# Kernel tuning notes

Hardware: AMD Instinct MI355X
Metric: run time of the kernel (lower is better)

## Reference

```python
import jax, jax.numpy as jnp
import numpy as np

B, N, M = 64, 256, 16
ONF, OEF = 92, 41
NF, EF = 128, 64
FINAL = 128  # final_node_len; final_layer outputs FINAL//2


def _linear_params(key, fan_in, fan_out):
    # kaiming_uniform fan_in, relu: bound = sqrt(6/fan_in)
    bound = np.sqrt(6.0 / fan_in)
    W = jax.random.uniform(key, (fan_out, fan_in), jnp.float32, -bound, bound)
    b = jnp.zeros((fan_out,), jnp.float32)
    return W, b


def setup_inputs() -> dict:
    key = jax.random.key(0)
    ks = jax.random.split(key, 12)
    node_fea = jax.random.normal(ks[0], (B, N, ONF), jnp.float32)
    edge_fea = jax.random.normal(ks[1], (B, N, M, OEF), jnp.float32)
    edge_fea_idx = jax.random.randint(ks[2], (B, N, M), 0, N)
    dis = jax.random.uniform(ks[3], (N, N), jnp.float32)
    Wn, bn = _linear_params(ks[4], ONF, NF)
    We, be = _linear_params(ks[5], OEF, EF)
    W1, b1 = _linear_params(ks[6], 2 * NF + EF, 2 * NF)
    W2, b2 = _linear_params(ks[7], 2 * NF + EF, 2 * NF)
    W3, b3 = _linear_params(ks[8], 2 * NF + EF, 2 * NF)
    Wf, bf = _linear_params(ks[9], NF, FINAL // 2)
    return dict(node_fea=node_fea, edge_fea=edge_fea, edge_fea_idx=edge_fea_idx,
                dis=dis, Wn=Wn, bn=bn, We=We, be=be,
                W1=W1, b1=b1, a1=jnp.float32(0.7),
                W2=W2, b2=b2, a2=jnp.float32(0.7),
                W3=W3, b3=b3, a3=jnp.float32(0.7),
                Wf=Wf, bf=bf,
                DAw=jnp.float32(48.0 / 5.0), DAb=jnp.float32(-28.0 / 5.0))


def _conv(nf, ef, idx, W, b, alpha):
    # nf: [B,N,F]; ef: [B,N,M,E]; idx: [B,N,M]
    Bb, Nn, Mm = idx.shape
    F = nf.shape[-1]
    idx_c = jnp.maximum(idx, 0)
    gathered = jax.vmap(lambda x, i: x[i])(nf, idx_c)           # [B,N,M,F]
    self_exp = jnp.broadcast_to(nf[:, :, None, :], (Bb, Nn, Mm, F))
    total = jnp.concatenate([self_exp, gathered, ef], axis=-1)   # [B,N,M,2F+E]
    gated = jnp.einsum('bnmi,oi->bnmo', total, W) + b            # [B,N,M,2F]
    nbr_filter, nbr_core = jnp.split(gated, 2, axis=-1)
    mask = (idx >= 0).astype(nf.dtype)[..., None]
    nbr_filter = jax.nn.sigmoid(nbr_filter) * mask
    nbr_core = jax.nn.softplus(nbr_core)
    nbr_sumed = jnp.sum(nbr_filter * nbr_core, axis=2)           # [B,N,F]
    return jax.nn.softplus(alpha * nf + nbr_sumed)


def reference(node_fea, edge_fea, edge_fea_idx, dis,
              Wn, bn, We, be,
              W1, b1, a1, W2, b2, a2, W3, b3, a3,
              Wf, bf, DAw, DAb):
    nf = node_fea @ Wn.T + bn                                    # [B,N,NF]
    ef = edge_fea @ We.T + be                                    # [B,N,M,EF]
    nf = _conv(nf, ef, edge_fea_idx, W1, b1, a1)
    nf = _conv(nf, ef, edge_fea_idx, W2, b2, a2)
    nf = _conv(nf, ef, edge_fea_idx, W3, b3, a3)
    nf = nf @ Wf.T + bf                                          # [B,N,FINAL//2]
    DA = jax.nn.sigmoid(DAw * dis + DAb)                         # [N,N]
    node1 = jnp.einsum('ij,bjf->bif', DA, nf)
    return jnp.concatenate([nf, node1], axis=2)                  # [B,N,FINAL]
```

## Files before the change

kernel.cpp:

```cpp
#include <hip/hip_runtime.h>
#include <hip/hip_bf16.h>
#include <math.h>

#define Bb   64
#define Nn   256
#define Mm   16
#define ONF  92
#define OEF  41
#define NF   128
#define EF   64
#define KDIM 320
#define ODIM 256
#define FINAL 128
#define K0C  6

typedef __attribute__((ext_vector_type(8))) short short8;
typedef __attribute__((ext_vector_type(4))) float f32x4;

__device__ __forceinline__ float sigmoidf_(float x) {
    float e = __expf(-x);
    return __builtin_amdgcn_rcpf(1.0f + e);
}
__device__ __forceinline__ float softplusf_(float x) {
    return fmaxf(x, 0.0f) + __logf(1.0f + __expf(-fabsf(x)));
}
__device__ __forceinline__ __hip_bfloat16 to_bf16(float x) { return __float2bfloat16(x); }

__global__ void k_transpose(const float* __restrict__ in, float* __restrict__ out, int O, int I)
{
    int t = blockIdx.x * 256 + threadIdx.x;
    if (t < O * I) {
        int o = t / I, i = t - o * I;
        out[i * O + o] = in[t];
    }
}

__global__ void k_wswz2(const float* __restrict__ in, __hip_bfloat16* __restrict__ out,
                        int O, int Itot, int koff, int Kuse, int K0)
{
    int t = blockIdx.x * 256 + threadIdx.x;
    int total = (O >> 4) * K0 * 512;
    if (t < total) {
        int j = t & 7;
        int u = t >> 3;
        int lane = u & 63;
        int ln16 = lane & 15, q = lane >> 4;
        int v = u >> 6;
        int k0 = v % K0, tile = v / K0;
        int n = tile * 16 + ln16, k = k0 * 32 + q * 8 + j;
        out[t] = (k < Kuse) ? to_bf16(in[(size_t)n * Itot + koff + k]) : to_bf16(0.0f);
    }
}

__global__ void k_da(const float* __restrict__ dis, const float* __restrict__ pw,
                     const float* __restrict__ pb, __hip_bfloat16* __restrict__ DAf)
{
    int t = blockIdx.x * 256 + threadIdx.x;
    if (t < Nn * Nn) {
        int i = t >> 8, jx = t & 255;
        float v = sigmoidf_(fmaf(*pw, dis[t], *pb));
        int itile = i >> 4, ln16 = i & 15;
        int k0 = jx >> 5, q = (jx >> 3) & 3, jj = jx & 7;
        DAf[(size_t)((((itile * 8 + k0) << 6) + (q << 4) + ln16)) * 8 + jj] = to_bf16(v);
    }
}

template<int KIN, int K0, int NCOLS>
__global__ __launch_bounds__(256) void k_emb(
    const float* __restrict__ X, const __hip_bfloat16* __restrict__ Bswz,
    const float* __restrict__ bias, __hip_bfloat16* __restrict__ Y)
{
    constexpr int KP = K0 * 32;
    constexpr int TPW = NCOLS / 64;
    constexpr int OLD = NCOLS + 24;
    __shared__ __align__(16) __hip_bfloat16 A_s[4 * K0 * 512];
    __shared__ __align__(16) __hip_bfloat16 O_s[64 * OLD];

    const int row0 = blockIdx.x * 64;
    const int t = threadIdx.x;

    {
        const float4* Xb = (const float4*)(X + (size_t)row0 * KIN);
        constexpr int NV = (64 * KIN) / 4;
        for (int c = t; c < NV; c += 256) {
            float4 v = Xb[c];
            int flat = c * 4;
            #pragma unroll
            for (int e = 0; e < 4; e++) {
                int f = flat + e;
                int row = f / KIN, k = f - row * KIN;
                int mt = row >> 4, ln16 = row & 15;
                int k0 = k >> 5, q = (k >> 3) & 3, j = k & 7;
                float vv = (e == 0) ? v.x : (e == 1) ? v.y : (e == 2) ? v.z : v.w;
                A_s[(((mt * K0 + k0) << 6) + (q << 4) + ln16) * 8 + j] = to_bf16(vv);
            }
        }
        constexpr int PAD = KP - KIN;
        for (int c = t; c < 64 * PAD; c += 256) {
            int row = c / PAD, k = KIN + (c - row * PAD);
            int mt = row >> 4, ln16 = row & 15;
            int k0 = k >> 5, q = (k >> 3) & 3, j = k & 7;
            A_s[(((mt * K0 + k0) << 6) + (q << 4) + ln16) * 8 + j] = to_bf16(0.0f);
        }
    }
    __syncthreads();

    const int wv = t >> 6, lane = t & 63;
    const int q = lane >> 4, ln16 = lane & 15;

    f32x4 acc[4][TPW];
    #pragma unroll
    for (int p = 0; p < TPW; p++) {
        float bv = bias[(wv * TPW + p) * 16 + ln16];
        #pragma unroll
        for (int mt = 0; mt < 4; mt++) acc[mt][p] = (f32x4){bv, bv, bv, bv};
    }

    short8 bw[TPW][K0];
    #pragma unroll
    for (int p = 0; p < TPW; p++)
        #pragma unroll
        for (int k0 = 0; k0 < K0; k0++)
            bw[p][k0] = *(const short8*)(Bswz + ((size_t)((wv * TPW + p) * K0 + k0) << 9) + (lane << 3));

    #pragma unroll
    for (int k0 = 0; k0 < K0; k0++) {
        short8 af[4];
        #pragma unroll
        for (int mt = 0; mt < 4; mt++)
            af[mt] = *(const short8*)(A_s + (((mt * K0 + k0) << 6) + lane) * 8);
        #pragma unroll
        for (int mt = 0; mt < 4; mt++)
            #pragma unroll
            for (int p = 0; p < TPW; p++)
                acc[mt][p] = __builtin_amdgcn_mfma_f32_16x16x32_bf16(af[mt], bw[p][k0], acc[mt][p], 0, 0, 0);
    }

    #pragma unroll
    for (int mt = 0; mt < 4; mt++)
        #pragma unroll
        for (int p = 0; p < TPW; p++) {
            int col = (wv * TPW + p) * 16 + ln16;
            #pragma unroll
            for (int r = 0; r < 4; r++)
                O_s[(mt * 16 + q * 4 + r) * OLD + col] = to_bf16(acc[mt][p][r]);
        }
    __syncthreads();
    constexpr int CH = NCOLS / 8;
    for (int c = t; c < 64 * CH; c += 256) {
        int row = c / CH, ch = c - row * CH;
        *(uint4*)(Y + (size_t)(row0 + row) * NCOLS + ch * 8) =
            *(const uint4*)(O_s + row * OLD + ch * 8);
    }
}

__global__ __launch_bounds__(256) void k_self(
    const __hip_bfloat16* __restrict__ nf,
    const __hip_bfloat16* __restrict__ Wsb,
    const float* __restrict__ bias,
    float* __restrict__ S)
{
    __shared__ __align__(16) __hip_bfloat16 A_s[16 * 512];
    const int row0 = blockIdx.x * 64;
    const int t = threadIdx.x;
    const int wv = t >> 6, lane = t & 63;
    const int q = lane >> 4, ln16 = lane & 15;

    const __hip_bfloat16* rowp = nf + (size_t)(row0 + (wv << 4) + ln16) * NF;
    #pragma unroll
    for (int k0 = 0; k0 < 4; k0++)
        *(uint4*)(A_s + ((wv * 4 + k0) * 64 + lane) * 8) =
            *(const uint4*)(rowp + k0 * 32 + q * 8);
    __syncthreads();

    f32x4 acc[4][4];
    #pragma unroll
    for (int p = 0; p < 4; p++) {
        float bv = bias[(wv * 4 + p) * 16 + ln16];
        #pragma unroll
        for (int mt = 0; mt < 4; mt++) acc[mt][p] = (f32x4){bv, bv, bv, bv};
    }

    #pragma unroll
    for (int k0 = 0; k0 < 4; k0++) {
        short8 af[4];
        #pragma unroll
        for (int mt = 0; mt < 4; mt++)
            af[mt] = *(const short8*)(A_s + ((mt * 4 + k0) * 64 + lane) * 8);
        #pragma unroll
        for (int p = 0; p < 4; p++) {
            short8 bw = *(const short8*)(Wsb + ((size_t)((wv * 4 + p) * 4 + k0) << 9) + (lane << 3));
            #pragma unroll
            for (int mt = 0; mt < 4; mt++)
                acc[mt][p] = __builtin_amdgcn_mfma_f32_16x16x32_bf16(af[mt], bw, acc[mt][p], 0, 0, 0);
        }
    }

    #pragma unroll
    for (int mt = 0; mt < 4; mt++)
        #pragma unroll
        for (int p = 0; p < 4; p++) {
            int col = (wv * 4 + p) * 16 + ln16;
            #pragma unroll
            for (int r = 0; r < 4; r++)
                S[(size_t)(row0 + mt * 16 + q * 4 + r) * ODIM + col] = acc[mt][p][r];
        }
}

template<bool PRECOMP>
__global__ __launch_bounds__(256, 4) void k_conv_mfma(
    const __hip_bfloat16* __restrict__ nf_in,
    const float* __restrict__ edge_fea,
    const __hip_bfloat16* __restrict__ ef_bf,
    const int*   __restrict__ eidx,
    const float* __restrict__ WeT,
    const float* __restrict__ be,
    const __hip_bfloat16* __restrict__ Wb,
    const float* __restrict__ S,
    const float* __restrict__ palpha,
    __hip_bfloat16* __restrict__ nf_out)
{
    __shared__ __align__(16) __hip_bfloat16 A_s[4 * K0C * 512];

    const int node0 = blockIdx.x * 4;
    const int b = node0 >> 8;
    const int t = threadIdx.x;
    const int wv = t >> 6, lane = t & 63;
    const int q = lane >> 4, ln16 = lane & 15;
    const int row = (wv << 4) + ln16;

    const int myidx = eidx[node0 * Mm + row];
    const unsigned long long mball = __ballot(eidx[node0 * Mm + lane] >= 0);

    f32x4 accF[4][2], accC[4][2];
    #pragma unroll
    for (int mt = 0; mt < 4; mt++) {
        const float* Sp = S + (size_t)(node0 + mt) * ODIM;
        #pragma unroll
        for (int p = 0; p < 2; p++) {
            int colF = (2 * wv + p) * 16 + ln16;
            float sF = Sp[colF], sC = Sp[colF + NF];
            accF[mt][p] = (f32x4){sF, sF, sF, sF};
            accC[mt][p] = (f32x4){sC, sC, sC, sC};
        }
    }

    {
        int j = myidx < 0 ? 0 : myidx;
        const __hip_bfloat16* gathp = nf_in + (size_t)((b << 8) + j) * NF;
        #pragma unroll
        for (int k0 = 0; k0 < 4; k0++)
            *(uint4*)(A_s + ((wv * K0C + k0) * 64 + lane) * 8) =
                *(const uint4*)(gathp + k0 * 32 + q * 8);
        if (PRECOMP) {
            const __hip_bfloat16* efp = ef_bf + (size_t)((node0 << 4) + row) * EF;
            #pragma unroll
            for (int k0 = 0; k0 < 2; k0++)
                *(uint4*)(A_s + ((wv * K0C + 4 + k0) * 64 + lane) * 8) =
                    *(const uint4*)(efp + k0 * 32 + q * 8);
        } else {
            for (int c = t; c < 64 * EF; c += 256) {
                int rr = c >> 6, col = c & 63;
                float a = be[col];
                const float* er = edge_fea + (size_t)(node0 * Mm + rr) * OEF;
                #pragma unroll
                for (int i = 0; i < OEF; i++) a = fmaf(er[i], WeT[i * EF + col], a);
                int mt = rr >> 4, l16 = rr & 15;
                int k0 = 4 + (col >> 5), qq = (col >> 3) & 3, jj = col & 7;
                A_s[((mt * K0C + k0) * 64 + qq * 16 + l16) * 8 + jj] = to_bf16(a);
            }
        }
    }
    __syncthreads();

    const __hip_bfloat16* WF0 = Wb + ((size_t)(2 * wv) * (K0C * 512)) + (lane << 3);
    const __hip_bfloat16* WF1 = WF0 + K0C * 512;
    const __hip_bfloat16* WC0 = WF0 + 8 * (K0C * 512);
    const __hip_bfloat16* WC1 = WC0 + K0C * 512;

    #pragma unroll
    for (int k0 = 0; k0 < K0C; k0++) {
        short8 cF0 = *(const short8*)(WF0 + k0 * 512);
        short8 cF1 = *(const short8*)(WF1 + k0 * 512);
        short8 cC0 = *(const short8*)(WC0 + k0 * 512);
        short8 cC1 = *(const short8*)(WC1 + k0 * 512);
        short8 af[4];
        #pragma unroll
        for (int mt = 0; mt < 4; mt++)
            af[mt] = *(const short8*)(A_s + ((mt * K0C + k0) * 64 + lane) * 8);
        #pragma unroll
        for (int mt = 0; mt < 4; mt++) {
            accF[mt][0] = __builtin_amdgcn_mfma_f32_16x16x32_bf16(af[mt], cF0, accF[mt][0], 0, 0, 0);
            accF[mt][1] = __builtin_amdgcn_mfma_f32_16x16x32_bf16(af[mt], cF1, accF[mt][1], 0, 0, 0);
            accC[mt][0] = __builtin_amdgcn_mfma_f32_16x16x32_bf16(af[mt], cC0, accC[mt][0], 0, 0, 0);
            accC[mt][1] = __builtin_amdgcn_mfma_f32_16x16x32_bf16(af[mt], cC1, accC[mt][1], 0, 0, 0);
        }
    }

    const float alpha = *palpha;
    #pragma unroll
    for (int mt = 0; mt < 4; mt++) {
        const int gnode = node0 + mt;
        #pragma unroll
        for (int p = 0; p < 2; p++) {
            float partial = 0.0f;
            #pragma unroll
            for (int r = 0; r < 4; r++) {
                bool msk = (mball >> (mt * 16 + q * 4 + r)) & 1ull;
                float f = sigmoidf_(accF[mt][p][r]);
                float c = softplusf_(accC[mt][p][r]);
                partial += msk ? f * c : 0.0f;
            }
            partial += __shfl_xor(partial, 16);
            partial += __shfl_xor(partial, 32);
            if (q == 0) {
                int col = (2 * wv + p) * 16 + ln16;
                float self = __bfloat162float(nf_in[(size_t)gnode * NF + col]);
                nf_out[(size_t)gnode * NF + col] = to_bf16(softplusf_(fmaf(alpha, self, partial)));
            }
        }
    }
}

__global__ __launch_bounds__(256) void k_final_mfma(
    const __hip_bfloat16* __restrict__ nf, const __hip_bfloat16* __restrict__ Wfb,
    const float* __restrict__ bfv, float* __restrict__ out,
    __hip_bfloat16* __restrict__ XT)
{
    __shared__ __align__(16) __hip_bfloat16 A_s[16 * 512];
    const int node0 = blockIdx.x * 64;
    const int bloc = node0 >> 8;
    const int t = threadIdx.x;
    const int wv = t >> 6, lane = t & 63;
    const int q = lane >> 4, ln16 = lane & 15;

    const __hip_bfloat16* rowp = nf + (size_t)(node0 + (wv << 4) + ln16) * NF;
    #pragma unroll
    for (int k0 = 0; k0 < 4; k0++)
        *(uint4*)(A_s + ((wv * 4 + k0) * 64 + lane) * 8) =
            *(const uint4*)(rowp + k0 * 32 + q * 8);
    __syncthreads();

    short8 bw[4];
    #pragma unroll
    for (int k0 = 0; k0 < 4; k0++)
        bw[k0] = *(const short8*)(Wfb + ((size_t)(wv * 4 + k0) * 64 + lane) * 8);

    float bv = bfv[wv * 16 + ln16];
    f32x4 acc[4];
    #pragma unroll
    for (int mt = 0; mt < 4; mt++) acc[mt] = (f32x4){bv, bv, bv, bv};

    #pragma unroll
    for (int k0 = 0; k0 < 4; k0++) {
        short8 af[4];
        #pragma unroll
        for (int mt = 0; mt < 4; mt++)
            af[mt] = *(const short8*)(A_s + ((mt * 4 + k0) * 64 + lane) * 8);
        #pragma unroll
        for (int mt = 0; mt < 4; mt++)
            acc[mt] = __builtin_amdgcn_mfma_f32_16x16x32_bf16(af[mt], bw[k0], acc[mt], 0, 0, 0);
    }

    const int col = (wv << 4) + ln16;
    #pragma unroll
    for (int mt = 0; mt < 4; mt++)
        #pragma unroll
        for (int r = 0; r < 4; r++) {
            int row = mt * 16 + q * 4 + r;
            float v = acc[mt][r];
            out[(size_t)(node0 + row) * FINAL + col] = v;
            XT[(size_t)(bloc * 64 + col) * 256 + (node0 & 255) + row] = to_bf16(v);
        }
}

__global__ __launch_bounds__(256) void k_node1_mfma(
    const __hip_bfloat16* __restrict__ DAf,
    const __hip_bfloat16* __restrict__ XT,
    float* __restrict__ out)
{
    __shared__ __align__(16) __hip_bfloat16 B_s[32 * 512];
    const int blk = blockIdx.x;
    const int b = blk >> 2, i0 = (blk & 3) * 64;
    const int t = threadIdx.x;
    const int wv = t >> 6, lane = t & 63;
    const int q = lane >> 4, ln16 = lane & 15;

    const __hip_bfloat16* xrow = XT + (size_t)(b * 64 + (wv << 4) + ln16) * 256;
    #pragma unroll
    for (int k0 = 0; k0 < 8; k0++)
        *(uint4*)(B_s + ((wv * 8 + k0) * 64 + lane) * 8) =
            *(const uint4*)(xrow + k0 * 32 + q * 8);
    __syncthreads();

    f32x4 acc[4];
    #pragma unroll
    for (int mt = 0; mt < 4; mt++) acc[mt] = (f32x4){0.f, 0.f, 0.f, 0.f};

    #pragma unroll
    for (int k0 = 0; k0 < 8; k0++) {
        short8 bfr = *(const short8*)(B_s + ((wv * 8 + k0) * 64 + lane) * 8);
        short8 af[4];
        #pragma unroll
        for (int mt = 0; mt < 4; mt++)
            af[mt] = *(const short8*)(DAf + (size_t)(((i0 >> 4) + mt) * 8 + k0) * 512 + (lane << 3));
        #pragma unroll
        for (int mt = 0; mt < 4; mt++)
            acc[mt] = __builtin_amdgcn_mfma_f32_16x16x32_bf16(af[mt], bfr, acc[mt], 0, 0, 0);
    }

    #pragma unroll
    for (int mt = 0; mt < 4; mt++)
        #pragma unroll
        for (int r = 0; r < 4; r++) {
            int i = i0 + mt * 16 + q * 4 + r;
            out[(size_t)((b << 8) + i) * FINAL + 64 + (wv << 4) + ln16] = acc[mt][r];
        }
}

extern "C" void kernel_launch(void* const* d_in, const int* in_sizes, int n_in,
                              void* d_out, int out_size, void* d_ws, size_t ws_size,
                              hipStream_t stream)
{
    const float* node_fea = (const float*)d_in[0];
    const float* edge_fea = (const float*)d_in[1];
    const int*   eidx     = (const int*)  d_in[2];
    const float* dis      = (const float*)d_in[3];
    const float* Wn = (const float*)d_in[4];
    const float* bn = (const float*)d_in[5];
    const float* We = (const float*)d_in[6];
    const float* be = (const float*)d_in[7];
    const float* W1 = (const float*)d_in[8];
    const float* b1 = (const float*)d_in[9];
    const float* a1 = (const float*)d_in[10];
    const float* W2 = (const float*)d_in[11];
    const float* b2 = (const float*)d_in[12];
    const float* a2 = (const float*)d_in[13];
    const float* W3 = (const float*)d_in[14];
    const float* b3 = (const float*)d_in[15];
    const float* a3 = (const float*)d_in[16];
    const float* Wf = (const float*)d_in[17];
    const float* bf = (const float*)d_in[18];
    const float* DAw = (const float*)d_in[19];
    const float* DAb = (const float*)d_in[20];
    float* out = (float*)d_out;

    char* base = (char*)d_ws;
    size_t off = 0;
    auto alloc = [&](size_t bytes) { char* p = base + off; off = (off + bytes + 255) & ~(size_t)255; return p; };
    __hip_bfloat16* nfA = (__hip_bfloat16*)alloc((size_t)Bb * Nn * NF * 2);
    __hip_bfloat16* nfB = (__hip_bfloat16*)alloc((size_t)Bb * Nn * NF * 2);
    __hip_bfloat16* W1b = (__hip_bfloat16*)alloc((size_t)16 * K0C * 512 * 2);
    __hip_bfloat16* W2b = (__hip_bfloat16*)alloc((size_t)16 * K0C * 512 * 2);
    __hip_bfloat16* W3b = (__hip_bfloat16*)alloc((size_t)16 * K0C * 512 * 2);
    __hip_bfloat16* W1s = (__hip_bfloat16*)alloc((size_t)16 * 4 * 512 * 2);
    __hip_bfloat16* W2s = (__hip_bfloat16*)alloc((size_t)16 * 4 * 512 * 2);
    __hip_bfloat16* W3s = (__hip_bfloat16*)alloc((size_t)16 * 4 * 512 * 2);
    float* WeT = (float*)alloc((size_t)OEF * EF * 4);
    __hip_bfloat16* DAf = (__hip_bfloat16*)alloc((size_t)Nn * Nn * 2);
    __hip_bfloat16* Wnb = (__hip_bfloat16*)alloc((size_t)(NF / 16) * 3 * 512 * 2);
    __hip_bfloat16* Web = (__hip_bfloat16*)alloc((size_t)(EF / 16) * 2 * 512 * 2);
    __hip_bfloat16* Wfb = (__hip_bfloat16*)alloc((size_t)(64 / 16) * 4 * 512 * 2);
    __hip_bfloat16* XT  = (__hip_bfloat16*)alloc((size_t)Bb * 64 * Nn * 2);
    float* S = (float*)alloc((size_t)Bb * Nn * ODIM * 4);
    __hip_bfloat16* efb = (__hip_bfloat16*)alloc((size_t)Bb * Nn * Mm * EF * 2);
    const bool precomp = (ws_size >= off);

    hipLaunchKernelGGL(k_transpose, dim3((EF * OEF + 255) / 256), dim3(256), 0, stream, We, WeT, EF, OEF);
    hipLaunchKernelGGL(k_wswz2, dim3((16 * K0C * 512 + 255) / 256), dim3(256), 0, stream, W1, W1b, ODIM, KDIM, NF, 192, K0C);
    hipLaunchKernelGGL(k_wswz2, dim3((16 * K0C * 512 + 255) / 256), dim3(256), 0, stream, W2, W2b, ODIM, KDIM, NF, 192, K0C);
    hipLaunchKernelGGL(k_wswz2, dim3((16 * K0C * 512 + 255) / 256), dim3(256), 0, stream, W3, W3b, ODIM, KDIM, NF, 192, K0C);
    hipLaunchKernelGGL(k_wswz2, dim3((16 * 4 * 512 + 255) / 256), dim3(256), 0, stream, W1, W1s, ODIM, KDIM, 0, NF, 4);
    hipLaunchKernelGGL(k_wswz2, dim3((16 * 4 * 512 + 255) / 256), dim3(256), 0, stream, W2, W2s, ODIM, KDIM, 0, NF, 4);
    hipLaunchKernelGGL(k_wswz2, dim3((16 * 4 * 512 + 255) / 256), dim3(256), 0, stream, W3, W3s, ODIM, KDIM, 0, NF, 4);
    hipLaunchKernelGGL(k_wswz2, dim3((8 * 3 * 512 + 255) / 256), dim3(256), 0, stream, Wn, Wnb, NF, ONF, 0, ONF, 3);
    hipLaunchKernelGGL(k_wswz2, dim3((4 * 2 * 512 + 255) / 256), dim3(256), 0, stream, We, Web, EF, OEF, 0, OEF, 2);
    hipLaunchKernelGGL(k_wswz2, dim3((4 * 4 * 512 + 255) / 256), dim3(256), 0, stream, Wf, Wfb, 64, NF, 0, NF, 4);
    hipLaunchKernelGGL(k_da, dim3((Nn * Nn + 255) / 256), dim3(256), 0, stream, dis, DAw, DAb, DAf);

    if (precomp)
        hipLaunchKernelGGL((k_emb<OEF, 2, EF>), dim3(Bb * Nn * Mm / 64), dim3(256), 0, stream,
                           edge_fea, Web, be, efb);
    hipLaunchKernelGGL((k_emb<ONF, 3, NF>), dim3(Bb * Nn / 64), dim3(256), 0, stream,
                       node_fea, Wnb, bn, nfA);

    const int NG = Bb * Nn / 64;
    if (precomp) {
        hipLaunchKernelGGL(k_self, dim3(NG), dim3(256), 0, stream, nfA, W1s, b1, S);
        hipLaunchKernelGGL((k_conv_mfma<true>), dim3(Bb * Nn / 4), dim3(256), 0, stream,
                           nfA, edge_fea, efb, eidx, WeT, be, W1b, S, a1, nfB);
        hipLaunchKernelGGL(k_self, dim3(NG), dim3(256), 0, stream, nfB, W2s, b2, S);
        hipLaunchKernelGGL((k_conv_mfma<true>), dim3(Bb * Nn / 4), dim3(256), 0, stream,
                           nfB, edge_fea, efb, eidx, WeT, be, W2b, S, a2, nfA);
        hipLaunchKernelGGL(k_self, dim3(NG), dim3(256), 0, stream, nfA, W3s, b3, S);
        hipLaunchKernelGGL((k_conv_mfma<true>), dim3(Bb * Nn / 4), dim3(256), 0, stream,
                           nfA, edge_fea, efb, eidx, WeT, be, W3b, S, a3, nfB);
    } else {
        hipLaunchKernelGGL(k_self, dim3(NG), dim3(256), 0, stream, nfA, W1s, b1, S);
        hipLaunchKernelGGL((k_conv_mfma<false>), dim3(Bb * Nn / 4), dim3(256), 0, stream,
                           nfA, edge_fea, efb, eidx, WeT, be, W1b, S, a1, nfB);
        hipLaunchKernelGGL(k_self, dim3(NG), dim3(256), 0, stream, nfB, W2s, b2, S);
        hipLaunchKernelGGL((k_conv_mfma<false>), dim3(Bb * Nn / 4), dim3(256), 0, stream,
                           nfB, edge_fea, efb, eidx, WeT, be, W2b, S, a2, nfA);
        hipLaunchKernelGGL(k_self, dim3(NG), dim3(256), 0, stream, nfA, W3s, b3, S);
        hipLaunchKernelGGL((k_conv_mfma<false>), dim3(Bb * Nn / 4), dim3(256), 0, stream,
                           nfA, edge_fea, efb, eidx, WeT, be, W3b, S, a3, nfB);
    }

    hipLaunchKernelGGL(k_final_mfma, dim3(Bb * Nn / 64), dim3(256), 0, stream, nfB, Wfb, bf, out, XT);
    hipLaunchKernelGGL(k_node1_mfma, dim3(Bb * 4), dim3(256), 0, stream, DAf, XT, out);
}
```

Measured before the change: 344.7 us.

## Fuse self-term GEMM into conv kernel and merge prep/embed launches

Removes the separate k_self kernel and its fp32 S buffer. Each conv block now computes its own 4 nodes' self-projection with extra MFMAs on a padded 16-row tile and broadcasts the results via shuffles. All weight-swizzle, transpose and DA prep kernels are merged into one k_prep launch, and the node and edge embedding kernels into one k_embed_all launch, which cuts launch count and S traffic. The self GEMM in conv uses only 4 of 16 MFMA rows, so it wastes compute, and launch bounds drop from 4 to 3 blocks per CU, which may reduce occupancy.

```diff
diff --git a/kernel.cpp b/kernel.cpp
--- a/kernel.cpp
+++ b/kernel.cpp
@@ -26,37 +26,65 @@
 }
 __device__ __forceinline__ __hip_bfloat16 to_bf16(float x) { return __float2bfloat16(x); }
 
-__global__ void k_transpose(const float* __restrict__ in, float* __restrict__ out, int O, int I)
+__device__ __forceinline__ void swz(const float* __restrict__ in, __hip_bfloat16* __restrict__ out,
+                                    int t, int Itot, int koff, int Kuse, int K0)
+{
+    int j = t & 7;
+    int u = t >> 3;
+    int lane = u & 63;
+    int ln16 = lane & 15, q = lane >> 4;
+    int v = u >> 6;
+    int k0 = v % K0, tile = v / K0;
+    int n = tile * 16 + ln16, k = k0 * 32 + q * 8 + j;
+    out[t] = (k < Kuse) ? to_bf16(in[(size_t)n * Itot + koff + k]) : to_bf16(0.0f);
+}
+
+#define SZ_WET (OEF * EF)
+#define SZ_WB  (16 * K0C * 512)
+#define SZ_WS  (16 * 4 * 512)
+#define SZ_WNB ((NF / 16) * 3 * 512)
+#define SZ_WEB ((EF / 16) * 2 * 512)
+#define SZ_WFB ((64 / 16) * 4 * 512)
+#define SZ_DA  (Nn * Nn)
+#define PREP_TOTAL (SZ_WET + 3 * SZ_WB + 3 * SZ_WS + SZ_WNB + SZ_WEB + SZ_WFB + SZ_DA)
+
+__global__ __launch_bounds__(256) void k_prep(
+    const float* __restrict__ We, const float* __restrict__ W1,
+    const float* __restrict__ W2, const float* __restrict__ W3,
+    const float* __restrict__ Wn, const float* __restrict__ Wf,
+    const float* __restrict__ dis, const float* __restrict__ pw, const float* __restrict__ pb,
+    float* __restrict__ WeT,
+    __hip_bfloat16* __restrict__ W1b, __hip_bfloat16* __restrict__ W2b, __hip_bfloat16* __restrict__ W3b,
+    __hip_bfloat16* __restrict__ W1s, __hip_bfloat16* __restrict__ W2s, __hip_bfloat16* __restrict__ W3s,
+    __hip_bfloat16* __restrict__ Wnb, __hip_bfloat16* __restrict__ Web, __hip_bfloat16* __restrict__ Wfb,
+    __hip_bfloat16* __restrict__ DAf)
 {
     int t = blockIdx.x * 256 + threadIdx.x;
-    if (t < O * I) {
-        int o = t / I, i = t - o * I;
-        out[i * O + o] = in[t];
-    }
-}
-
-__global__ void k_wswz2(const float* __restrict__ in, __hip_bfloat16* __restrict__ out,
-                        int O, int Itot, int koff, int Kuse, int K0)
-{
-    int t = blockIdx.x * 256 + threadIdx.x;
-    int total = (O >> 4) * K0 * 512;
-    if (t < total) {
-        int j = t & 7;
-        int u = t >> 3;
-        int lane = u & 63;
-        int ln16 = lane & 15, q = lane >> 4;
-        int v = u >> 6;
-        int k0 = v % K0, tile = v / K0;
-        int n = tile * 16 + ln16, k = k0 * 32 + q * 8 + j;
-        out[t] = (k < Kuse) ? to_bf16(in[(size_t)n * Itot + koff + k]) : to_bf16(0.0f);
-    }
-}
-
-__global__ void k_da(const float* __restrict__ dis, const float* __restrict__ pw,
-                     const float* __restrict__ pb, __hip_bfloat16* __restrict__ DAf)
-{
-    int t = blockIdx.x * 256 + threadIdx.x;
-    if (t < Nn * Nn) {
+    if (t < SZ_WET) {
+        int o = t / OEF, i = t - o * OEF;
+        WeT[i * EF + o] = We[t];
+        return;
+    }
+    t -= SZ_WET;
+    if (t < SZ_WB) { swz(W1, W1b, t, KDIM, NF, 192, K0C); return; }
+    t -= SZ_WB;
+    if (t < SZ_WB) { swz(W2, W2b, t, KDIM, NF, 192, K0C); return; }
+    t -= SZ_WB;
+    if (t < SZ_WB) { swz(W3, W3b, t, KDIM, NF, 192, K0C); return; }
+    t -= SZ_WB;
+    if (t < SZ_WS) { swz(W1, W1s, t, KDIM, 0, NF, 4); return; }
+    t -= SZ_WS;
+    if (t < SZ_WS) { swz(W2, W2s, t, KDIM, 0, NF, 4); return; }
+    t -= SZ_WS;
+    if (t < SZ_WS) { swz(W3, W3s, t, KDIM, 0, NF, 4); return; }
+    t -= SZ_WS;
+    if (t < SZ_WNB) { swz(Wn, Wnb, t, ONF, 0, ONF, 3); return; }
+    t -= SZ_WNB;
+    if (t < SZ_WEB) { swz(We, Web, t, OEF, 0, OEF, 2); return; }
+    t -= SZ_WEB;
+    if (t < SZ_WFB) { swz(Wf, Wfb, t, NF, 0, NF, 4); return; }
+    t -= SZ_WFB;
+    if (t < SZ_DA) {
         int i = t >> 8, jx = t & 255;
         float v = sigmoidf_(fmaf(*pw, dis[t], *pb));
         int itile = i >> 4, ln16 = i & 15;
@@ -66,17 +94,16 @@
 }
 
 template<int KIN, int K0, int NCOLS>
-__global__ __launch_bounds__(256) void k_emb(
-    const float* __restrict__ X, const __hip_bfloat16* __restrict__ Bswz,
-    const float* __restrict__ bias, __hip_bfloat16* __restrict__ Y)
+__device__ __forceinline__ void emb_body(
+    int bid, const float* __restrict__ X, const __hip_bfloat16* __restrict__ Bswz,
+    const float* __restrict__ bias, __hip_bfloat16* __restrict__ Y,
+    __hip_bfloat16* A_s, __hip_bfloat16* O_s)
 {
     constexpr int KP = K0 * 32;
     constexpr int TPW = NCOLS / 64;
     constexpr int OLD = NCOLS + 24;
-    __shared__ __align__(16) __hip_bfloat16 A_s[4 * K0 * 512];
-    __shared__ __align__(16) __hip_bfloat16 O_s[64 * OLD];
-
-    const int row0 = blockIdx.x * 64;
+
+    const int row0 = bid * 64;
     const int t = threadIdx.x;
 
     {
@@ -154,61 +181,22 @@
     }
 }
 
-__global__ __launch_bounds__(256) void k_self(
-    const __hip_bfloat16* __restrict__ nf,
-    const __hip_bfloat16* __restrict__ Wsb,
-    const float* __restrict__ bias,
-    float* __restrict__ S)
-{
-    __shared__ __align__(16) __hip_bfloat16 A_s[16 * 512];
-    const int row0 = blockIdx.x * 64;
-    const int t = threadIdx.x;
-    const int wv = t >> 6, lane = t & 63;
-    const int q = lane >> 4, ln16 = lane & 15;
-
-    const __hip_bfloat16* rowp = nf + (size_t)(row0 + (wv << 4) + ln16) * NF;
-    #pragma unroll
-    for (int k0 = 0; k0 < 4; k0++)
-        *(uint4*)(A_s + ((wv * 4 + k0) * 64 + lane) * 8) =
-            *(const uint4*)(rowp + k0 * 32 + q * 8);
-    __syncthreads();
-
-    f32x4 acc[4][4];
-    #pragma unroll
-    for (int p = 0; p < 4; p++) {
-        float bv = bias[(wv * 4 + p) * 16 + ln16];
-        #pragma unroll
-        for (int mt = 0; mt < 4; mt++) acc[mt][p] = (f32x4){bv, bv, bv, bv};
-    }
-
-    #pragma unroll
-    for (int k0 = 0; k0 < 4; k0++) {
-        short8 af[4];
-        #pragma unroll
-        for (int mt = 0; mt < 4; mt++)
-            af[mt] = *(const short8*)(A_s + ((mt * 4 + k0) * 64 + lane) * 8);
-        #pragma unroll
-        for (int p = 0; p < 4; p++) {
-            short8 bw = *(const short8*)(Wsb + ((size_t)((wv * 4 + p) * 4 + k0) << 9) + (lane << 3));
-            #pragma unroll
-            for (int mt = 0; mt < 4; mt++)
-                acc[mt][p] = __builtin_amdgcn_mfma_f32_16x16x32_bf16(af[mt], bw, acc[mt][p], 0, 0, 0);
-        }
-    }
-
-    #pragma unroll
-    for (int mt = 0; mt < 4; mt++)
-        #pragma unroll
-        for (int p = 0; p < 4; p++) {
-            int col = (wv * 4 + p) * 16 + ln16;
-            #pragma unroll
-            for (int r = 0; r < 4; r++)
-                S[(size_t)(row0 + mt * 16 + q * 4 + r) * ODIM + col] = acc[mt][p][r];
-        }
+__global__ __launch_bounds__(256) void k_embed_all(
+    const float* __restrict__ node_fea, const __hip_bfloat16* __restrict__ Wnb,
+    const float* __restrict__ bn, __hip_bfloat16* __restrict__ nf0,
+    const float* __restrict__ edge_fea, const __hip_bfloat16* __restrict__ Web,
+    const float* __restrict__ be, __hip_bfloat16* __restrict__ efb)
+{
+    __shared__ __align__(16) __hip_bfloat16 A_s[4 * 3 * 512];
+    __shared__ __align__(16) __hip_bfloat16 O_s[64 * (NF + 24)];
+    if (blockIdx.x < 256)
+        emb_body<ONF, 3, NF>(blockIdx.x, node_fea, Wnb, bn, nf0, A_s, O_s);
+    else
+        emb_body<OEF, 2, EF>(blockIdx.x - 256, edge_fea, Web, be, efb, A_s, O_s);
 }
 
 template<bool PRECOMP>
-__global__ __launch_bounds__(256, 4) void k_conv_mfma(
+__global__ __launch_bounds__(256, 3) void k_conv_mfma(
     const __hip_bfloat16* __restrict__ nf_in,
     const float* __restrict__ edge_fea,
     const __hip_bfloat16* __restrict__ ef_bf,
@@ -216,11 +204,13 @@
     const float* __restrict__ WeT,
     const float* __restrict__ be,
     const __hip_bfloat16* __restrict__ Wb,
-    const float* __restrict__ S,
+    const __hip_bfloat16* __restrict__ Wsb,
+    const float* __restrict__ bias,
     const float* __restrict__ palpha,
     __hip_bfloat16* __restrict__ nf_out)
 {
     __shared__ __align__(16) __hip_bfloat16 A_s[4 * K0C * 512];
+    __shared__ __align__(16) __hip_bfloat16 A_sf[4 * 512];
 
     const int node0 = blockIdx.x * 4;
     const int b = node0 >> 8;
@@ -232,19 +222,6 @@
     const int myidx = eidx[node0 * Mm + row];
     const unsigned long long mball = __ballot(eidx[node0 * Mm + lane] >= 0);
 
-    f32x4 accF[4][2], accC[4][2];
-    #pragma unroll
-    for (int mt = 0; mt < 4; mt++) {
-        const float* Sp = S + (size_t)(node0 + mt) * ODIM;
-        #pragma unroll
-        for (int p = 0; p < 2; p++) {
-            int colF = (2 * wv + p) * 16 + ln16;
-            float sF = Sp[colF], sC = Sp[colF + NF];
-            accF[mt][p] = (f32x4){sF, sF, sF, sF};
-            accC[mt][p] = (f32x4){sC, sC, sC, sC};
-        }
-    }
-
     {
         int j = myidx < 0 ? 0 : myidx;
         const __hip_bfloat16* gathp = nf_in + (size_t)((b << 8) + j) * NF;
@@ -252,6 +229,9 @@
         for (int k0 = 0; k0 < 4; k0++)
             *(uint4*)(A_s + ((wv * K0C + k0) * 64 + lane) * 8) =
                 *(const uint4*)(gathp + k0 * 32 + q * 8);
+        if (lane < 16)
+            *(uint4*)(A_sf + (((lane >> 2) * 64) + (lane & 3) * 16 + wv) * 8) =
+                *(const uint4*)(nf_in + (size_t)(node0 + wv) * NF + lane * 8);
         if (PRECOMP) {
             const __hip_bfloat16* efp = ef_bf + (size_t)((node0 << 4) + row) * EF;
             #pragma unroll
@@ -272,6 +252,36 @@
         }
     }
     __syncthreads();
+
+    f32x4 sv[4];
+    #pragma unroll
+    for (int c = 0; c < 4; c++) {
+        int tile = 2 * wv + (c & 1) + ((c >> 1) << 3);
+        float bv = bias[tile * 16 + ln16];
+        sv[c] = (f32x4){bv, bv, bv, bv};
+    }
+    #pragma unroll
+    for (int k0 = 0; k0 < 4; k0++) {
+        short8 afs = *(const short8*)(A_sf + (k0 * 64 + lane) * 8);
+        #pragma unroll
+        for (int c = 0; c < 4; c++) {
+            int tile = 2 * wv + (c & 1) + ((c >> 1) << 3);
+            short8 bws = *(const short8*)(Wsb + ((size_t)(tile * 4 + k0) << 9) + (lane << 3));
+            sv[c] = __builtin_amdgcn_mfma_f32_16x16x32_bf16(afs, bws, sv[c], 0, 0, 0);
+        }
+    }
+
+    f32x4 accF[4][2], accC[4][2];
+    #pragma unroll
+    for (int mt = 0; mt < 4; mt++) {
+        #pragma unroll
+        for (int p = 0; p < 2; p++) {
+            float vF = __shfl(sv[p][mt], ln16);
+            float vC = __shfl(sv[2 + p][mt], ln16);
+            accF[mt][p] = (f32x4){vF, vF, vF, vF};
+            accC[mt][p] = (f32x4){vC, vC, vC, vC};
+        }
+    }
 
     const __hip_bfloat16* WF0 = Wb + ((size_t)(2 * wv) * (K0C * 512)) + (lane << 3);
     const __hip_bfloat16* WF1 = WF0 + K0C * 512;
@@ -450,61 +460,42 @@
     auto alloc = [&](size_t bytes) { char* p = base + off; off = (off + bytes + 255) & ~(size_t)255; return p; };
     __hip_bfloat16* nfA = (__hip_bfloat16*)alloc((size_t)Bb * Nn * NF * 2);
     __hip_bfloat16* nfB = (__hip_bfloat16*)alloc((size_t)Bb * Nn * NF * 2);
-    __hip_bfloat16* W1b = (__hip_bfloat16*)alloc((size_t)16 * K0C * 512 * 2);
-    __hip_bfloat16* W2b = (__hip_bfloat16*)alloc((size_t)16 * K0C * 512 * 2);
-    __hip_bfloat16* W3b = (__hip_bfloat16*)alloc((size_t)16 * K0C * 512 * 2);
-    __hip_bfloat16* W1s = (__hip_bfloat16*)alloc((size_t)16 * 4 * 512 * 2);
-    __hip_bfloat16* W2s = (__hip_bfloat16*)alloc((size_t)16 * 4 * 512 * 2);
-    __hip_bfloat16* W3s = (__hip_bfloat16*)alloc((size_t)16 * 4 * 512 * 2);
+    __hip_bfloat16* W1b = (__hip_bfloat16*)alloc((size_t)SZ_WB * 2);
+    __hip_bfloat16* W2b = (__hip_bfloat16*)alloc((size_t)SZ_WB * 2);
+    __hip_bfloat16* W3b = (__hip_bfloat16*)alloc((size_t)SZ_WB * 2);
+    __hip_bfloat16* W1s = (__hip_bfloat16*)alloc((size_t)SZ_WS * 2);
+    __hip_bfloat16* W2s = (__hip_bfloat16*)alloc((size_t)SZ_WS * 2);
+    __hip_bfloat16* W3s = (__hip_bfloat16*)alloc((size_t)SZ_WS * 2);
     float* WeT = (float*)alloc((size_t)OEF * EF * 4);
     __hip_bfloat16* DAf = (__hip_bfloat16*)alloc((size_t)Nn * Nn * 2);
-    __hip_bfloat16* Wnb = (__hip_bfloat16*)alloc((size_t)(NF / 16) * 3 * 512 * 2);
-    __hip_bfloat16* Web = (__hip_bfloat16*)alloc((size_t)(EF / 16) * 2 * 512 * 2);
-    __hip_bfloat16* Wfb = (__hip_bfloat16*)alloc((size_t)(64 / 16) * 4 * 512 * 2);
+    __hip_bfloat16* Wnb = (__hip_bfloat16*)alloc((size_t)SZ_WNB * 2);
+    __hip_bfloat16* Web = (__hip_bfloat16*)alloc((size_t)SZ_WEB * 2);
+    __hip_bfloat16* Wfb = (__hip_bfloat16*)alloc((size_t)SZ_WFB * 2);
     __hip_bfloat16* XT  = (__hip_bfloat16*)alloc((size_t)Bb * 64 * Nn * 2);
-    float* S = (float*)alloc((size_t)Bb * Nn * ODIM * 4);
     __hip_bfloat16* efb = (__hip_bfloat16*)alloc((size_t)Bb * Nn * Mm * EF * 2);
     const bool precomp = (ws_size >= off);
 
-    hipLaunchKernelGGL(k_transpose, dim3((EF * OEF + 255) / 256), dim3(256), 0, stream, We, WeT, EF, OEF);
-    hipLaunchKernelGGL(k_wswz2, dim3((16 * K0C * 512 + 255) / 256), dim3(256), 0, stream, W1, W1b, ODIM, KDIM, NF, 192, K0C);
-    hipLaunchKernelGGL(k_wswz2, dim3((16 * K0C * 512 + 255) / 256), dim3(256), 0, stream, W2, W2b, ODIM, KDIM, NF, 192, K0C);
-    hipLaunchKernelGGL(k_wswz2, dim3((16 * K0C * 512 + 255) / 256), dim3(256), 0, stream, W3, W3b, ODIM, KDIM, NF, 192, K0C);
-    hipLaunchKernelGGL(k_wswz2, dim3((16 * 4 * 512 + 255) / 256), dim3(256), 0, stream, W1, W1s, ODIM, KDIM, 0, NF, 4);
-    hipLaunchKernelGGL(k_wswz2, dim3((16 * 4 * 512 + 255) / 256), dim3(256), 0, stream, W2, W2s, ODIM, KDIM, 0, NF, 4);
-    hipLaunchKernelGGL(k_wswz2, dim3((16 * 4 * 512 + 255) / 256), dim3(256), 0, stream, W3, W3s, ODIM, KDIM, 0, NF, 4);
-    hipLaunchKernelGGL(k_wswz2, dim3((8 * 3 * 512 + 255) / 256), dim3(256), 0, stream, Wn, Wnb, NF, ONF, 0, ONF, 3);
-    hipLaunchKernelGGL(k_wswz2, dim3((4 * 2 * 512 + 255) / 256), dim3(256), 0, stream, We, Web, EF, OEF, 0, OEF, 2);
-    hipLaunchKernelGGL(k_wswz2, dim3((4 * 4 * 512 + 255) / 256), dim3(256), 0, stream, Wf, Wfb, 64, NF, 0, NF, 4);
-    hipLaunchKernelGGL(k_da, dim3((Nn * Nn + 255) / 256), dim3(256), 0, stream, dis, DAw, DAb, DAf);
-
-    if (precomp)
-        hipLaunchKernelGGL((k_emb<OEF, 2, EF>), dim3(Bb * Nn * Mm / 64), dim3(256), 0, stream,
-                           edge_fea, Web, be, efb);
-    hipLaunchKernelGGL((k_emb<ONF, 3, NF>), dim3(Bb * Nn / 64), dim3(256), 0, stream,
-                       node_fea, Wnb, bn, nfA);
-
-    const int NG = Bb * Nn / 64;
+    hipLaunchKernelGGL(k_prep, dim3((PREP_TOTAL + 255) / 256), dim3(256), 0, stream,
+                       We, W1, W2, W3, Wn, Wf, dis, DAw, DAb,
+                       WeT, W1b, W2b, W3b, W1s, W2s, W3s, Wnb, Web, Wfb, DAf);
+
+    hipLaunchKernelGGL(k_embed_all, dim3(precomp ? (256 + Bb * Nn * Mm / 64) : 256), dim3(256), 0, stream,
+                       node_fea, Wnb, bn, nfA, edge_fea, Web, be, efb);
+
     if (precomp) {
-        hipLaunchKernelGGL(k_self, dim3(NG), dim3(256), 0, stream, nfA, W1s, b1, S);
         hipLaunchKernelGGL((k_conv_mfma<true>), dim3(Bb * Nn / 4), dim3(256), 0, stream,
-                           nfA, edge_fea, efb, eidx, WeT, be, W1b, S, a1, nfB);
-        hipLaunchKernelGGL(k_self, dim3(NG), dim3(256), 0, stream, nfB, W2s, b2, S);
+                           nfA, edge_fea, efb, eidx, WeT, be, W1b, W1s, b1, a1, nfB);
         hipLaunchKernelGGL((k_conv_mfma<true>), dim3(Bb * Nn / 4), dim3(256), 0, stream,
-                           nfB, edge_fea, efb, eidx, WeT, be, W2b, S, a2, nfA);
-        hipLaunchKernelGGL(k_self, dim3(NG), dim3(256), 0, stream, nfA, W3s, b3, S);
+                           nfB, edge_fea, efb, eidx, WeT, be, W2b, W2s, b2, a2, nfA);
         hipLaunchKernelGGL((k_conv_mfma<true>), dim3(Bb * Nn / 4), dim3(256), 0, stream,
-                           nfA, edge_fea, efb, eidx, WeT, be, W3b, S, a3, nfB);
+                           nfA, edge_fea, efb, eidx, WeT, be, W3b, W3s, b3, a3, nfB);
     } else {
-        hipLaunchKernelGGL(k_self, dim3(NG), dim3(256), 0, stream, nfA, W1s, b1, S);
         hipLaunchKernelGGL((k_conv_mfma<false>), dim3(Bb * Nn / 4), dim3(256), 0, stream,
-                           nfA, edge_fea, efb, eidx, WeT, be, W1b, S, a1, nfB);
-        hipLaunchKernelGGL(k_self, dim3(NG), dim3(256), 0, stream, nfB, W2s, b2, S);
+                           nfA, edge_fea, efb, eidx, WeT, be, W1b, W1s, b1, a1, nfB);
         hipLaunchKernelGGL((k_conv_mfma<false>), dim3(Bb * Nn / 4), dim3(256), 0, stream,
-                           nfB, edge_fea, efb, eidx, WeT, be, W2b, S, a2, nfA);
-        hipLaunchKernelGGL(k_self, dim3(NG), dim3(256), 0, stream, nfA, W3s, b3, S);
+                           nfB, edge_fea, efb, eidx, WeT, be, W2b, W2s, b2, a2, nfA);
         hipLaunchKernelGGL((k_conv_mfma<false>), dim3(Bb * Nn / 4), dim3(256), 0, stream,
-                           nfA, edge_fea, efb, eidx, WeT, be, W3b, S, a3, nfB);
+                           nfA, edge_fea, efb, eidx, WeT, be, W3b, W3s, b3, a3, nfB);
     }
 
     hipLaunchKernelGGL(k_final_mfma, dim3(Bb * Nn / 64), dim3(256), 0, stream, nfB, Wfb, bf, out, XT);
```

After: 308.8 us. 10.4% less time.
